# Performance work log

Measured on AMD Instinct MI355X. Metric: run time of the kernel, lower is better.

## Reference

```python
import jax, jax.numpy as jnp
import numpy as np

N, T, DYN, STAT, H = 50000, 24, 16, 8, 64
E = 1_600_000


def gru_last(x, Wih, Whh, bih, bhh):
    # x: [N, T, DYN]; torch GRU gate order: r, z, n
    gx = jnp.einsum('ntd,gd->ntg', x, Wih) + bih  # [N, T, 3H]
    h0 = jnp.zeros((x.shape[0], H), x.dtype)

    def step(h, gx_t):
        gh = h @ Whh.T + bhh  # [N, 3H]
        xr, xz, xn = jnp.split(gx_t, 3, axis=-1)
        hr, hz, hn = jnp.split(gh, 3, axis=-1)
        r = jax.nn.sigmoid(xr + hr)
        z = jax.nn.sigmoid(xz + hz)
        n = jnp.tanh(xn + r * hn)
        h_new = (1.0 - z) * n + z * h
        return h_new, None

    h_last, _ = jax.lax.scan(step, h0, jnp.swapaxes(gx, 0, 1))  # scan over T
    return h_last  # [N, H]


def gcn_layer(x, W, b, src, dst, w):
    h = x @ W  # [N, out]
    msg = h[src] * w[:, None]  # gather + weight  [E, out]
    agg = jax.ops.segment_sum(msg, dst, num_segments=N)  # scatter-add
    return agg + b


def setup_inputs() -> dict:
    key = jax.random.key(0)
    ks = jax.random.split(key, 16)
    s = 0.1
    return {
        'x_dyn': jax.random.normal(ks[0], (N, T, DYN), jnp.float32),
        'x_stat': jax.random.normal(ks[1], (N, STAT), jnp.float32),
        'edge_index': jax.random.randint(ks[2], (2, E), 0, N, jnp.int32),
        'edge_weight': jax.random.uniform(ks[3], (E,), jnp.float32),
        'Wih': jax.random.normal(ks[4], (3 * H, DYN), jnp.float32) * s,
        'Whh': jax.random.normal(ks[5], (3 * H, H), jnp.float32) * s,
        'bih': jnp.zeros((3 * H,), jnp.float32),
        'bhh': jnp.zeros((3 * H,), jnp.float32),
        'W1': jax.random.normal(ks[6], (H + STAT, H), jnp.float32) * s,
        'b1': jnp.zeros((H,), jnp.float32),
        'W2': jax.random.normal(ks[7], (H, H), jnp.float32) * s,
        'b2': jnp.zeros((H,), jnp.float32),
        'Wa': jax.random.normal(ks[8], (H, 1), jnp.float32) * s,
        'ba': jnp.zeros((1,), jnp.float32),
        'Wp': jax.random.normal(ks[9], (H, 1), jnp.float32) * s,
        'bp': jnp.zeros((1,), jnp.float32),
    }


def reference(x_dyn, x_stat, edge_index, edge_weight,
              Wih, Whh, bih, bhh, W1, b1, W2, b2, Wa, ba, Wp, bp):
    src, dst = edge_index[0], edge_index[1]
    z = gru_last(x_dyn, Wih, Whh, bih, bhh)            # [N, H]
    h = jnp.concatenate([z, x_stat], axis=1)           # [N, H+STAT]
    h = jax.nn.relu(gcn_layer(h, W1, b1, src, dst, edge_weight))
    h = jax.nn.relu(gcn_layer(h, W2, b2, src, dst, edge_weight))
    # dropout omitted (eval mode)
    aqi = (h @ Wa + ba)[:, 0]
    pm = (h @ Wp + bp)[:, 0]
    return aqi, pm
```

## Files before the change

### kernel.cpp

```cpp
#include <hip/hip_runtime.h>
#include <cstdint>
#include <cstddef>

#define NNODES 50000
#define TT 24
#define DYNF 16
#define STATF 8
#define HDIM 64
#define NEDGES 1600000
#define NB 32
#define GRU_BLOCKS ((NNODES + NB - 1) / NB)
#define FILL_CHUNK 1024
#define FILL_CHUNKS ((NEDGES + FILL_CHUNK - 1) / FILL_CHUNK)
#define CAP 80
#define SLICE (NNODES / 8)
#define BINCAP 210000
#define STAGE 192

typedef __attribute__((ext_vector_type(8))) short bf16x8;
typedef __attribute__((ext_vector_type(4))) float f32x4;
typedef __attribute__((ext_vector_type(2))) float f32x2;
typedef __attribute__((ext_vector_type(2))) unsigned u32x2;

__device__ __forceinline__ unsigned short f2bf(float f) {
    unsigned u = __float_as_uint(f);
    u = (u + 0x7FFFu + ((u >> 16) & 1u)) >> 16;
    return (unsigned short)u;
}
__device__ __forceinline__ float bf2f(unsigned short s) {
    return __uint_as_float((unsigned)s << 16);
}
__device__ __forceinline__ bf16x8 cvt8(const float* __restrict__ p) {
    bf16x8 r;
    #pragma unroll
    for (int i = 0; i < 8; ++i) r[i] = (short)f2bf(p[i]);
    return r;
}
__device__ __forceinline__ bf16x8 zero8() {
    bf16x8 z;
    #pragma unroll
    for (int i = 0; i < 8; ++i) z[i] = 0;
    return z;
}
__device__ __forceinline__ float fast_tanh(float x) {
    float e = __expf(2.f * x);
    return 1.f - 2.f * __builtin_amdgcn_rcpf(e + 1.f);
}

__global__ __launch_bounds__(256, 4) void gru_fill_kernel(
    const float* __restrict__ x_dyn, const float* __restrict__ x_stat,
    const float* __restrict__ Wih, const float* __restrict__ Whh,
    const float* __restrict__ bih, const float* __restrict__ bhh,
    const float* __restrict__ W1, unsigned short* __restrict__ t1,
    const int* __restrict__ srcv, const int* __restrict__ dstv,
    const float* __restrict__ ew, int* __restrict__ binCnt,
    u32x2* __restrict__ bins)
{
    constexpr int S_H = 72;
    constexpr int S_X = 40;
    __shared__ short hbuf[2][NB * S_H];
    __shared__ short xbuf[2][NB * S_X];
    __shared__ u32x2 stg[8][STAGE];
    __shared__ int lcnt[8];
    __shared__ int gbase[8];

    const int tid = (int)threadIdx.x;

    if ((int)blockIdx.x >= GRU_BLOCKS) {
        const int fb = (int)blockIdx.x - GRU_BLOCKS;
        const int base = fb * FILL_CHUNK;
        if (tid < 8) lcnt[tid] = 0;
        __syncthreads();
        #pragma unroll
        for (int j = 0; j < FILL_CHUNK / 256; ++j) {
            const int e = base + j * 256 + tid;
            if (e < NEDGES) {
                const int d = __builtin_nontemporal_load(dstv + e);
                const int s = __builtin_nontemporal_load(srcv + e);
                const float we = __builtin_nontemporal_load(ew + e);
                const int b = d / SLICE;
                u32x2 rec;
                rec[0] = (unsigned)s | ((unsigned)f2bf(we) << 16);
                rec[1] = (unsigned)(d - b * SLICE);
                const int pos = atomicAdd(&lcnt[b], 1);
                if (pos < STAGE) {
                    stg[b][pos] = rec;
                } else {
                    const int gp = atomicAdd(&binCnt[b], 1);
                    if (gp < BINCAP) bins[(size_t)b * BINCAP + gp] = rec;
                }
            }
        }
        __syncthreads();
        if (tid < 8) {
            const int n = min(lcnt[tid], STAGE);
            gbase[tid] = atomicAdd(&binCnt[tid], n);
        }
        __syncthreads();
        #pragma unroll 1
        for (int b = 0; b < 8; ++b) {
            const int n = min(lcnt[b], STAGE);
            const int gb = gbase[b];
            for (int i = tid; i < n; i += 256)
                if (gb + i < BINCAP)
                    bins[(size_t)b * BINCAP + gb + i] = stg[b][i];
        }
        return;
    }

    const int lane = tid & 63;
    const int w = __builtin_amdgcn_readfirstlane(tid >> 6);
    const int col = lane & 15;
    const int quad = lane >> 4;
    const int node0 = (int)blockIdx.x * NB;

    bf16x8 Bh[3][2];
    bf16x8 Bx[3];
    #pragma unroll
    for (int g = 0; g < 3; ++g) {
        const int n = (w + g * 4) * 16 + col;
        #pragma unroll
        for (int kt = 0; kt < 2; ++kt)
            Bh[g][kt] = cvt8(Whh + (size_t)n * HDIM + kt * 32 + quad * 8);
        Bx[g] = (quad < 2) ? cvt8(Wih + (size_t)n * DYNF + quad * 8) : zero8();
    }

    const int jg = w * 16 + col;
    const float b_r  = bih[jg]        + bhh[jg];
    const float b_z  = bih[HDIM + jg] + bhh[HDIM + jg];
    const float b_xn = bih[2 * HDIM + jg];
    const float b_hn = bhh[2 * HDIM + jg];

    for (int i = tid; i < NB * S_H; i += 256) hbuf[0][i] = 0;

    auto stage_x = [&](int t, int b) {
        const int nd = tid >> 3, c = tid & 7;
        int node = node0 + nd;
        if (node >= NNODES) node = 0;
        const f32x2 v = __builtin_nontemporal_load(
            reinterpret_cast<const f32x2*>(
                x_dyn + (size_t)node * (TT * DYNF) + t * DYNF + c * 2));
        unsigned pk = (unsigned)f2bf(v[0]) | ((unsigned)f2bf(v[1]) << 16);
        *reinterpret_cast<unsigned*>(&xbuf[b][nd * S_X + c * 2]) = pk;
        *reinterpret_cast<unsigned*>(&xbuf[b][nd * S_X + 16 + c * 2]) = 0u;
    };
    stage_x(0, 0);

    float hprev[2][4];
    #pragma unroll
    for (int mt = 0; mt < 2; ++mt)
        #pragma unroll
        for (int r = 0; r < 4; ++r) hprev[mt][r] = 0.f;

    for (int t = 0; t < TT; ++t) {
        const int rb = t & 1;
        __syncthreads();

        f32x4 accr[2], accz[2], accnh[2], accnx[2];
        #pragma unroll
        for (int mt = 0; mt < 2; ++mt) {
            const int nd = mt * 16 + col;
            const bf16x8 a0 = *reinterpret_cast<const bf16x8*>(&hbuf[rb][nd * S_H + quad * 8]);
            const bf16x8 a1 = *reinterpret_cast<const bf16x8*>(&hbuf[rb][nd * S_H + 32 + quad * 8]);
            const bf16x8 ax = *reinterpret_cast<const bf16x8*>(&xbuf[rb][nd * S_X + quad * 8]);
            const f32x4 z4 = {0.f, 0.f, 0.f, 0.f};
            accr[mt]  = __builtin_amdgcn_mfma_f32_16x16x32_bf16(a0, Bh[0][0], z4, 0, 0, 0);
            accr[mt]  = __builtin_amdgcn_mfma_f32_16x16x32_bf16(a1, Bh[0][1], accr[mt], 0, 0, 0);
            accr[mt]  = __builtin_amdgcn_mfma_f32_16x16x32_bf16(ax, Bx[0],    accr[mt], 0, 0, 0);
            accz[mt]  = __builtin_amdgcn_mfma_f32_16x16x32_bf16(a0, Bh[1][0], z4, 0, 0, 0);
            accz[mt]  = __builtin_amdgcn_mfma_f32_16x16x32_bf16(a1, Bh[1][1], accz[mt], 0, 0, 0);
            accz[mt]  = __builtin_amdgcn_mfma_f32_16x16x32_bf16(ax, Bx[1],    accz[mt], 0, 0, 0);
            accnh[mt] = __builtin_amdgcn_mfma_f32_16x16x32_bf16(a0, Bh[2][0], z4, 0, 0, 0);
            accnh[mt] = __builtin_amdgcn_mfma_f32_16x16x32_bf16(a1, Bh[2][1], accnh[mt], 0, 0, 0);
            accnx[mt] = __builtin_amdgcn_mfma_f32_16x16x32_bf16(ax, Bx[2],    z4, 0, 0, 0);
        }

        if (t + 1 < TT) stage_x(t + 1, rb ^ 1);

        #pragma unroll
        for (int mt = 0; mt < 2; ++mt) {
            #pragma unroll
            for (int r = 0; r < 4; ++r) {
                const float dr = 1.f + __expf(-(accr[mt][r] + b_r));
                const float dz = 1.f + __expf(-(accz[mt][r] + b_z));
                const float q  = __builtin_amdgcn_rcpf(dr * dz);
                const float R  = q * dz;
                const float Z  = q * dr;
                const float Nn = fast_tanh(accnx[mt][r] + b_xn + R * (accnh[mt][r] + b_hn));
                const float hn = Nn + Z * (hprev[mt][r] - Nn);
                hprev[mt][r] = hn;
                hbuf[rb ^ 1][(mt * 16 + quad * 4 + r) * S_H + jg] = (short)f2bf(hn);
            }
        }
    }
    __syncthreads();

    bf16x8 Bw0, Bw1, Bw2;
    #pragma unroll
    for (int j = 0; j < 8; ++j) {
        Bw0[j] = (short)f2bf(W1[(size_t)(quad * 8 + j) * HDIM + jg]);
        Bw1[j] = (short)f2bf(W1[(size_t)(32 + quad * 8 + j) * HDIM + jg]);
    }
    if (quad == 0) {
        #pragma unroll
        for (int j = 0; j < 8; ++j)
            Bw2[j] = (short)f2bf(W1[(size_t)(HDIM + j) * HDIM + jg]);
    } else {
        Bw2 = zero8();
    }

    #pragma unroll
    for (int mt = 0; mt < 2; ++mt) {
        const int nd = mt * 16 + col;
        const bf16x8 a0 = *reinterpret_cast<const bf16x8*>(&hbuf[0][nd * S_H + quad * 8]);
        const bf16x8 a1 = *reinterpret_cast<const bf16x8*>(&hbuf[0][nd * S_H + 32 + quad * 8]);
        bf16x8 axs;
        if (quad == 0) {
            int node = node0 + nd;
            if (node >= NNODES) node = 0;
            axs = cvt8(x_stat + (size_t)node * STATF);
        } else {
            axs = zero8();
        }
        const f32x4 z4 = {0.f, 0.f, 0.f, 0.f};
        f32x4 aw;
        aw = __builtin_amdgcn_mfma_f32_16x16x32_bf16(a0, Bw0, z4, 0, 0, 0);
        aw = __builtin_amdgcn_mfma_f32_16x16x32_bf16(a1, Bw1, aw, 0, 0, 0);
        aw = __builtin_amdgcn_mfma_f32_16x16x32_bf16(axs, Bw2, aw, 0, 0, 0);
        #pragma unroll
        for (int r = 0; r < 4; ++r) {
            const int node = node0 + mt * 16 + quad * 4 + r;
            if (node < NNODES) t1[(size_t)node * HDIM + jg] = f2bf(aw[r]);
        }
    }
}

__global__ __launch_bounds__(256) void fill_scatter_kernel(
    const u32x2* __restrict__ bins, const int* __restrict__ binCnt,
    int* __restrict__ cursor, unsigned* __restrict__ csr)
{
    const int slice = (int)blockIdx.x & 7;
    const int sub   = (int)blockIdx.x >> 3;
    const int lo    = slice * SLICE;
    const int cnt   = min(binCnt[slice], BINCAP);
    const u32x2* __restrict__ mybin = bins + (size_t)slice * BINCAP;
    for (int i = sub * 256 + (int)threadIdx.x; i < cnt; i += 96 * 256) {
        const u32x2 r = __builtin_nontemporal_load(mybin + i);
        const int d = lo + (int)r[1];
        const int pos = atomicAdd(&cursor[d], 1);
        if (pos < CAP) csr[(size_t)d * CAP + pos] = r[0];
    }
}

__global__ __launch_bounds__(256) void gather_transform_kernel(
    const unsigned short* __restrict__ tsrc, const int* __restrict__ cursor,
    const unsigned* __restrict__ csr, const float* __restrict__ b1,
    const float* __restrict__ W2, unsigned short* __restrict__ out)
{
    __shared__ float aggL[16][68];
    const int tid  = (int)threadIdx.x;
    const int lane = tid & 63;
    const int w    = tid >> 6;
    const int q    = lane >> 4;
    const int f    = lane & 15;
    const int col  = lane & 15;
    const int quad = lane >> 4;
    const int node0 = (int)blockIdx.x * 16;
    const int jg = w * 16 + col;

    bf16x8 Bw0, Bw1;
    float bk0[8], bk1[8];
    #pragma unroll
    for (int j = 0; j < 8; ++j) {
        Bw0[j] = (short)f2bf(W2[(size_t)(quad * 8 + j) * HDIM + jg]);
        Bw1[j] = (short)f2bf(W2[(size_t)(32 + quad * 8 + j) * HDIM + jg]);
        bk0[j] = b1[quad * 8 + j];
        bk1[j] = b1[32 + quad * 8 + j];
    }

    for (int i = 0; i < 4; ++i) {
        const int nloc = w * 4 + i;
        const int node = node0 + nloc;
        const int beg = node * CAP;
        const int cnt = min(cursor[node], CAP);
        const int end = beg + cnt;
        float a0 = 0.f, a1 = 0.f, a2 = 0.f, a3 = 0.f;
        int p = beg;
        for (; p + 8 <= end; p += 8) {
            const unsigned e0 = csr[p + q];
            const unsigned e1 = csr[p + 4 + q];
            const u32x2 r0 = *reinterpret_cast<const u32x2*>(
                tsrc + (size_t)(e0 & 0xFFFFu) * HDIM + 4 * f);
            const u32x2 r1 = *reinterpret_cast<const u32x2*>(
                tsrc + (size_t)(e1 & 0xFFFFu) * HDIM + 4 * f);
            const float w0 = __uint_as_float(e0 & 0xFFFF0000u);
            const float w1 = __uint_as_float(e1 & 0xFFFF0000u);
            a0 += w0 * bf2f((unsigned short)(r0[0] & 0xFFFFu));
            a1 += w0 * bf2f((unsigned short)(r0[0] >> 16));
            a2 += w0 * bf2f((unsigned short)(r0[1] & 0xFFFFu));
            a3 += w0 * bf2f((unsigned short)(r0[1] >> 16));
            a0 += w1 * bf2f((unsigned short)(r1[0] & 0xFFFFu));
            a1 += w1 * bf2f((unsigned short)(r1[0] >> 16));
            a2 += w1 * bf2f((unsigned short)(r1[1] & 0xFFFFu));
            a3 += w1 * bf2f((unsigned short)(r1[1] >> 16));
        }
        if (p + 4 <= end) {
            const unsigned e0 = csr[p + q];
            const u32x2 r0 = *reinterpret_cast<const u32x2*>(
                tsrc + (size_t)(e0 & 0xFFFFu) * HDIM + 4 * f);
            const float w0 = __uint_as_float(e0 & 0xFFFF0000u);
            a0 += w0 * bf2f((unsigned short)(r0[0] & 0xFFFFu));
            a1 += w0 * bf2f((unsigned short)(r0[0] >> 16));
            a2 += w0 * bf2f((unsigned short)(r0[1] & 0xFFFFu));
            a3 += w0 * bf2f((unsigned short)(r0[1] >> 16));
            p += 4;
        }
        const int rem = end - p;
        if (q < rem) {
            const unsigned e0 = csr[p + q];
            const u32x2 r0 = *reinterpret_cast<const u32x2*>(
                tsrc + (size_t)(e0 & 0xFFFFu) * HDIM + 4 * f);
            const float w0 = __uint_as_float(e0 & 0xFFFF0000u);
            a0 += w0 * bf2f((unsigned short)(r0[0] & 0xFFFFu));
            a1 += w0 * bf2f((unsigned short)(r0[0] >> 16));
            a2 += w0 * bf2f((unsigned short)(r0[1] & 0xFFFFu));
            a3 += w0 * bf2f((unsigned short)(r0[1] >> 16));
        }
        a0 += __shfl_xor(a0, 16, 64); a0 += __shfl_xor(a0, 32, 64);
        a1 += __shfl_xor(a1, 16, 64); a1 += __shfl_xor(a1, 32, 64);
        a2 += __shfl_xor(a2, 16, 64); a2 += __shfl_xor(a2, 32, 64);
        a3 += __shfl_xor(a3, 16, 64); a3 += __shfl_xor(a3, 32, 64);
        if (lane < 16) {
            f32x4 o; o[0] = a0; o[1] = a1; o[2] = a2; o[3] = a3;
            *reinterpret_cast<f32x4*>(&aggL[nloc][4 * f]) = o;
        }
    }
    __syncthreads();

    bf16x8 fa0, fa1;
    #pragma unroll
    for (int j = 0; j < 8; ++j) {
        fa0[j] = (short)f2bf(fmaxf(aggL[col][quad * 8 + j] + bk0[j], 0.f));
        fa1[j] = (short)f2bf(fmaxf(aggL[col][32 + quad * 8 + j] + bk1[j], 0.f));
    }
    const f32x4 z4 = {0.f, 0.f, 0.f, 0.f};
    f32x4 aw;
    aw = __builtin_amdgcn_mfma_f32_16x16x32_bf16(fa0, Bw0, z4, 0, 0, 0);
    aw = __builtin_amdgcn_mfma_f32_16x16x32_bf16(fa1, Bw1, aw, 0, 0, 0);
    #pragma unroll
    for (int r = 0; r < 4; ++r)
        out[(size_t)(node0 + quad * 4 + r) * HDIM + jg] = f2bf(aw[r]);
}

__global__ __launch_bounds__(256) void gather_head_kernel(
    const unsigned short* __restrict__ tsrc, const int* __restrict__ cursor,
    const unsigned* __restrict__ csr,
    const float* __restrict__ b2, const float* __restrict__ Wa,
    const float* __restrict__ ba, const float* __restrict__ Wp,
    const float* __restrict__ bp, float* __restrict__ out)
{
    const int node = blockIdx.x * 4 + (threadIdx.x >> 6);
    const int lane = (int)threadIdx.x & 63;
    const int q = lane >> 4;
    const int f = lane & 15;
    if (node >= NNODES) return;
    const int beg = node * CAP;
    const int cnt = min(cursor[node], CAP);
    const int end = beg + cnt;
    float a0 = 0.f, a1 = 0.f, a2 = 0.f, a3 = 0.f;
    int p = beg;
    for (; p + 8 <= end; p += 8) {
        const unsigned e0 = csr[p + q];
        const unsigned e1 = csr[p + 4 + q];
        const u32x2 r0 = *reinterpret_cast<const u32x2*>(
            tsrc + (size_t)(e0 & 0xFFFFu) * HDIM + 4 * f);
        const u32x2 r1 = *reinterpret_cast<const u32x2*>(
            tsrc + (size_t)(e1 & 0xFFFFu) * HDIM + 4 * f);
        const float w0 = __uint_as_float(e0 & 0xFFFF0000u);
        const float w1 = __uint_as_float(e1 & 0xFFFF0000u);
        a0 += w0 * bf2f((unsigned short)(r0[0] & 0xFFFFu));
        a1 += w0 * bf2f((unsigned short)(r0[0] >> 16));
        a2 += w0 * bf2f((unsigned short)(r0[1] & 0xFFFFu));
        a3 += w0 * bf2f((unsigned short)(r0[1] >> 16));
        a0 += w1 * bf2f((unsigned short)(r1[0] & 0xFFFFu));
        a1 += w1 * bf2f((unsigned short)(r1[0] >> 16));
        a2 += w1 * bf2f((unsigned short)(r1[1] & 0xFFFFu));
        a3 += w1 * bf2f((unsigned short)(r1[1] >> 16));
    }
    if (p + 4 <= end) {
        const unsigned e0 = csr[p + q];
        const u32x2 r0 = *reinterpret_cast<const u32x2*>(
            tsrc + (size_t)(e0 & 0xFFFFu) * HDIM + 4 * f);
        const float w0 = __uint_as_float(e0 & 0xFFFF0000u);
        a0 += w0 * bf2f((unsigned short)(r0[0] & 0xFFFFu));
        a1 += w0 * bf2f((unsigned short)(r0[0] >> 16));
        a2 += w0 * bf2f((unsigned short)(r0[1] & 0xFFFFu));
        a3 += w0 * bf2f((unsigned short)(r0[1] >> 16));
        p += 4;
    }
    const int rem = end - p;
    if (q < rem) {
        const unsigned e0 = csr[p + q];
        const u32x2 r0 = *reinterpret_cast<const u32x2*>(
            tsrc + (size_t)(e0 & 0xFFFFu) * HDIM + 4 * f);
        const float w0 = __uint_as_float(e0 & 0xFFFF0000u);
        a0 += w0 * bf2f((unsigned short)(r0[0] & 0xFFFFu));
        a1 += w0 * bf2f((unsigned short)(r0[0] >> 16));
        a2 += w0 * bf2f((unsigned short)(r0[1] & 0xFFFFu));
        a3 += w0 * bf2f((unsigned short)(r0[1] >> 16));
    }
    a0 += __shfl_xor(a0, 16, 64); a0 += __shfl_xor(a0, 32, 64);
    a1 += __shfl_xor(a1, 16, 64); a1 += __shfl_xor(a1, 32, 64);
    a2 += __shfl_xor(a2, 16, 64); a2 += __shfl_xor(a2, 32, 64);
    a3 += __shfl_xor(a3, 16, 64); a3 += __shfl_xor(a3, 32, 64);

    const f32x4 bb = *reinterpret_cast<const f32x4*>(b2 + 4 * f);
    const f32x4 wa = *reinterpret_cast<const f32x4*>(Wa + 4 * f);
    const f32x4 wp = *reinterpret_cast<const f32x4*>(Wp + 4 * f);
    const float h0 = fmaxf(a0 + bb[0], 0.f);
    const float h1 = fmaxf(a1 + bb[1], 0.f);
    const float h2 = fmaxf(a2 + bb[2], 0.f);
    const float h3 = fmaxf(a3 + bb[3], 0.f);
    float sa = h0 * wa[0] + h1 * wa[1] + h2 * wa[2] + h3 * wa[3];
    float sp = h0 * wp[0] + h1 * wp[1] + h2 * wp[2] + h3 * wp[3];
    #pragma unroll
    for (int off = 1; off < 16; off <<= 1) {
        sa += __shfl_xor(sa, off, 64);
        sp += __shfl_xor(sp, off, 64);
    }
    if (lane == 0) {
        out[node] = sa + ba[0];
        out[NNODES + node] = sp + bp[0];
    }
}

extern "C" void kernel_launch(void* const* d_in, const int* in_sizes, int n_in,
                              void* d_out, int out_size, void* d_ws, size_t ws_size,
                              hipStream_t stream)
{
    const float* x_dyn  = (const float*)d_in[0];
    const float* x_stat = (const float*)d_in[1];
    const int*   eidx   = (const int*)  d_in[2];
    const float* ew     = (const float*)d_in[3];
    const float* Wih    = (const float*)d_in[4];
    const float* Whh    = (const float*)d_in[5];
    const float* bih    = (const float*)d_in[6];
    const float* bhh    = (const float*)d_in[7];
    const float* W1     = (const float*)d_in[8];
    const float* b1     = (const float*)d_in[9];
    const float* W2     = (const float*)d_in[10];
    const float* b2     = (const float*)d_in[11];
    const float* Wa     = (const float*)d_in[12];
    const float* ba     = (const float*)d_in[13];
    const float* Wp     = (const float*)d_in[14];
    const float* bp     = (const float*)d_in[15];

    const int* srcv = eidx;
    const int* dstv = eidx + NEDGES;

    unsigned short* t1 = (unsigned short*)d_ws;
    unsigned short* t2 = t1 + (size_t)NNODES * HDIM;
    unsigned* csr = (unsigned*)(t2 + (size_t)NNODES * HDIM);
    int* cursor = (int*)(csr + (size_t)NNODES * CAP);
    int* binCnt = cursor + NNODES;
    u32x2* bins = (u32x2*)(binCnt + 16);

    dim3 blk(256);

    hipMemsetAsync(cursor, 0, (size_t)(NNODES + 16) * sizeof(int), stream);

    gru_fill_kernel<<<dim3(GRU_BLOCKS + FILL_CHUNKS), blk, 0, stream>>>(
        x_dyn, x_stat, Wih, Whh, bih, bhh, W1, t1,
        srcv, dstv, ew, binCnt, bins);

    fill_scatter_kernel<<<dim3(8 * 96), blk, 0, stream>>>(
        bins, binCnt, cursor, csr);

    gather_transform_kernel<<<dim3(NNODES / 16), blk, 0, stream>>>(
        t1, cursor, csr, b1, W2, t2);

    gather_head_kernel<<<dim3((NNODES + 3) / 4), blk, 0, stream>>>(
        t2, cursor, csr, b2, Wa, ba, Wp, bp, (float*)d_out);
}
```

Baseline: 376.9 us.

## Overlap CSR scatter with GRU and interleave four nodes per wave in gathers

The edge binning now runs as its own kernel first. The per-node CSR scatter is fused into the GRU kernel as extra blocks, so the scatter overlaps the recurrent compute instead of the binning. Both gather kernels now handle four nodes per wave at once, issuing four independent csr and feature loads per iteration to hide latency. This costs some wasted lanes on inactive nodes and more registers, and the head kernel now processes 16 nodes per block.

```diff
diff --git a/kernel.cpp b/kernel.cpp
--- a/kernel.cpp
+++ b/kernel.cpp
@@ -16,6 +16,7 @@
 #define SLICE (NNODES / 8)
 #define BINCAP 210000
 #define STAGE 192
+#define SCAT_BLOCKS 768
 
 typedef __attribute__((ext_vector_type(8))) short bf16x8;
 typedef __attribute__((ext_vector_type(4))) float f32x4;
@@ -47,63 +48,81 @@
     return 1.f - 2.f * __builtin_amdgcn_rcpf(e + 1.f);
 }
 
-__global__ __launch_bounds__(256, 4) void gru_fill_kernel(
+__global__ __launch_bounds__(256) void fill_bin_kernel(
+    const int* __restrict__ srcv, const int* __restrict__ dstv,
+    const float* __restrict__ ew, int* __restrict__ binCnt,
+    u32x2* __restrict__ bins)
+{
+    __shared__ u32x2 stg[8][STAGE];
+    __shared__ int lcnt[8];
+    __shared__ int gbase[8];
+    const int tid = (int)threadIdx.x;
+    const int base = (int)blockIdx.x * FILL_CHUNK;
+    if (tid < 8) lcnt[tid] = 0;
+    __syncthreads();
+    #pragma unroll
+    for (int j = 0; j < FILL_CHUNK / 256; ++j) {
+        const int e = base + j * 256 + tid;
+        if (e < NEDGES) {
+            const int d = __builtin_nontemporal_load(dstv + e);
+            const int s = __builtin_nontemporal_load(srcv + e);
+            const float we = __builtin_nontemporal_load(ew + e);
+            const int b = d / SLICE;
+            u32x2 rec;
+            rec[0] = (unsigned)s | ((unsigned)f2bf(we) << 16);
+            rec[1] = (unsigned)(d - b * SLICE);
+            const int pos = atomicAdd(&lcnt[b], 1);
+            if (pos < STAGE) {
+                stg[b][pos] = rec;
+            } else {
+                const int gp = atomicAdd(&binCnt[b], 1);
+                if (gp < BINCAP) bins[(size_t)b * BINCAP + gp] = rec;
+            }
+        }
+    }
+    __syncthreads();
+    if (tid < 8) {
+        const int n = min(lcnt[tid], STAGE);
+        gbase[tid] = atomicAdd(&binCnt[tid], n);
+    }
+    __syncthreads();
+    #pragma unroll 1
+    for (int b = 0; b < 8; ++b) {
+        const int n = min(lcnt[b], STAGE);
+        const int gb = gbase[b];
+        for (int i = tid; i < n; i += 256)
+            if (gb + i < BINCAP)
+                bins[(size_t)b * BINCAP + gb + i] = stg[b][i];
+    }
+}
+
+__global__ __launch_bounds__(256, 4) void gru_scatter_kernel(
     const float* __restrict__ x_dyn, const float* __restrict__ x_stat,
     const float* __restrict__ Wih, const float* __restrict__ Whh,
     const float* __restrict__ bih, const float* __restrict__ bhh,
     const float* __restrict__ W1, unsigned short* __restrict__ t1,
-    const int* __restrict__ srcv, const int* __restrict__ dstv,
-    const float* __restrict__ ew, int* __restrict__ binCnt,
-    u32x2* __restrict__ bins)
+    const u32x2* __restrict__ bins, const int* __restrict__ binCnt,
+    int* __restrict__ cursor, unsigned* __restrict__ csr)
 {
     constexpr int S_H = 72;
     constexpr int S_X = 40;
     __shared__ short hbuf[2][NB * S_H];
     __shared__ short xbuf[2][NB * S_X];
-    __shared__ u32x2 stg[8][STAGE];
-    __shared__ int lcnt[8];
-    __shared__ int gbase[8];
 
     const int tid = (int)threadIdx.x;
 
     if ((int)blockIdx.x >= GRU_BLOCKS) {
         const int fb = (int)blockIdx.x - GRU_BLOCKS;
-        const int base = fb * FILL_CHUNK;
-        if (tid < 8) lcnt[tid] = 0;
-        __syncthreads();
-        #pragma unroll
-        for (int j = 0; j < FILL_CHUNK / 256; ++j) {
-            const int e = base + j * 256 + tid;
-            if (e < NEDGES) {
-                const int d = __builtin_nontemporal_load(dstv + e);
-                const int s = __builtin_nontemporal_load(srcv + e);
-                const float we = __builtin_nontemporal_load(ew + e);
-                const int b = d / SLICE;
-                u32x2 rec;
-                rec[0] = (unsigned)s | ((unsigned)f2bf(we) << 16);
-                rec[1] = (unsigned)(d - b * SLICE);
-                const int pos = atomicAdd(&lcnt[b], 1);
-                if (pos < STAGE) {
-                    stg[b][pos] = rec;
-                } else {
-                    const int gp = atomicAdd(&binCnt[b], 1);
-                    if (gp < BINCAP) bins[(size_t)b * BINCAP + gp] = rec;
-                }
-            }
-        }
-        __syncthreads();
-        if (tid < 8) {
-            const int n = min(lcnt[tid], STAGE);
-            gbase[tid] = atomicAdd(&binCnt[tid], n);
-        }
-        __syncthreads();
-        #pragma unroll 1
-        for (int b = 0; b < 8; ++b) {
-            const int n = min(lcnt[b], STAGE);
-            const int gb = gbase[b];
-            for (int i = tid; i < n; i += 256)
-                if (gb + i < BINCAP)
-                    bins[(size_t)b * BINCAP + gb + i] = stg[b][i];
+        const int slice = fb & 7;
+        const int sub   = fb >> 3;
+        const int lo    = slice * SLICE;
+        const int cnt   = min(binCnt[slice], BINCAP);
+        const u32x2* __restrict__ mybin = bins + (size_t)slice * BINCAP;
+        for (int i = sub * 256 + tid; i < cnt; i += (SCAT_BLOCKS / 8) * 256) {
+            const u32x2 r = __builtin_nontemporal_load(mybin + i);
+            const int d = lo + (int)r[1];
+            const int pos = atomicAdd(&cursor[d], 1);
+            if (pos < CAP) csr[(size_t)d * CAP + pos] = r[0];
         }
         return;
     }
@@ -235,23 +254,6 @@
     }
 }
 
-__global__ __launch_bounds__(256) void fill_scatter_kernel(
-    const u32x2* __restrict__ bins, const int* __restrict__ binCnt,
-    int* __restrict__ cursor, unsigned* __restrict__ csr)
-{
-    const int slice = (int)blockIdx.x & 7;
-    const int sub   = (int)blockIdx.x >> 3;
-    const int lo    = slice * SLICE;
-    const int cnt   = min(binCnt[slice], BINCAP);
-    const u32x2* __restrict__ mybin = bins + (size_t)slice * BINCAP;
-    for (int i = sub * 256 + (int)threadIdx.x; i < cnt; i += 96 * 256) {
-        const u32x2 r = __builtin_nontemporal_load(mybin + i);
-        const int d = lo + (int)r[1];
-        const int pos = atomicAdd(&cursor[d], 1);
-        if (pos < CAP) csr[(size_t)d * CAP + pos] = r[0];
-    }
-}
-
 __global__ __launch_bounds__(256) void gather_transform_kernel(
     const unsigned short* __restrict__ tsrc, const int* __restrict__ cursor,
     const unsigned* __restrict__ csr, const float* __restrict__ b1,
@@ -263,76 +265,74 @@
     const int w    = tid >> 6;
     const int q    = lane >> 4;
     const int f    = lane & 15;
-    const int col  = lane & 15;
-    const int quad = lane >> 4;
     const int node0 = (int)blockIdx.x * 16;
-    const int jg = w * 16 + col;
+    const int jg = w * 16 + f;
 
     bf16x8 Bw0, Bw1;
     float bk0[8], bk1[8];
     #pragma unroll
     for (int j = 0; j < 8; ++j) {
-        Bw0[j] = (short)f2bf(W2[(size_t)(quad * 8 + j) * HDIM + jg]);
-        Bw1[j] = (short)f2bf(W2[(size_t)(32 + quad * 8 + j) * HDIM + jg]);
-        bk0[j] = b1[quad * 8 + j];
-        bk1[j] = b1[32 + quad * 8 + j];
-    }
-
-    for (int i = 0; i < 4; ++i) {
-        const int nloc = w * 4 + i;
-        const int node = node0 + nloc;
-        const int beg = node * CAP;
+        Bw0[j] = (short)f2bf(W2[(size_t)(q * 8 + j) * HDIM + jg]);
+        Bw1[j] = (short)f2bf(W2[(size_t)(32 + q * 8 + j) * HDIM + jg]);
+        bk0[j] = b1[q * 8 + j];
+        bk1[j] = b1[32 + q * 8 + j];
+    }
+
+    int pn[4], en[4], bg[4];
+    float a[4][4];
+    #pragma unroll
+    for (int n = 0; n < 4; ++n) {
+        const int node = node0 + w * 4 + n;
+        bg[n] = node * CAP;
         const int cnt = min(cursor[node], CAP);
-        const int end = beg + cnt;
-        float a0 = 0.f, a1 = 0.f, a2 = 0.f, a3 = 0.f;
-        int p = beg;
-        for (; p + 8 <= end; p += 8) {
-            const unsigned e0 = csr[p + q];
-            const unsigned e1 = csr[p + 4 + q];
-            const u32x2 r0 = *reinterpret_cast<const u32x2*>(
-                tsrc + (size_t)(e0 & 0xFFFFu) * HDIM + 4 * f);
-            const u32x2 r1 = *reinterpret_cast<const u32x2*>(
-                tsrc + (size_t)(e1 & 0xFFFFu) * HDIM + 4 * f);
-            const float w0 = __uint_as_float(e0 & 0xFFFF0000u);
-            const float w1 = __uint_as_float(e1 & 0xFFFF0000u);
-            a0 += w0 * bf2f((unsigned short)(r0[0] & 0xFFFFu));
-            a1 += w0 * bf2f((unsigned short)(r0[0] >> 16));
-            a2 += w0 * bf2f((unsigned short)(r0[1] & 0xFFFFu));
-            a3 += w0 * bf2f((unsigned short)(r0[1] >> 16));
-            a0 += w1 * bf2f((unsigned short)(r1[0] & 0xFFFFu));
-            a1 += w1 * bf2f((unsigned short)(r1[0] >> 16));
-            a2 += w1 * bf2f((unsigned short)(r1[1] & 0xFFFFu));
-            a3 += w1 * bf2f((unsigned short)(r1[1] >> 16));
-        }
-        if (p + 4 <= end) {
-            const unsigned e0 = csr[p + q];
-            const u32x2 r0 = *reinterpret_cast<const u32x2*>(
-                tsrc + (size_t)(e0 & 0xFFFFu) * HDIM + 4 * f);
-            const float w0 = __uint_as_float(e0 & 0xFFFF0000u);
-            a0 += w0 * bf2f((unsigned short)(r0[0] & 0xFFFFu));
-            a1 += w0 * bf2f((unsigned short)(r0[0] >> 16));
-            a2 += w0 * bf2f((unsigned short)(r0[1] & 0xFFFFu));
-            a3 += w0 * bf2f((unsigned short)(r0[1] >> 16));
-            p += 4;
-        }
-        const int rem = end - p;
-        if (q < rem) {
-            const unsigned e0 = csr[p + q];
-            const u32x2 r0 = *reinterpret_cast<const u32x2*>(
-                tsrc + (size_t)(e0 & 0xFFFFu) * HDIM + 4 * f);
-            const float w0 = __uint_as_float(e0 & 0xFFFF0000u);
-            a0 += w0 * bf2f((unsigned short)(r0[0] & 0xFFFFu));
-            a1 += w0 * bf2f((unsigned short)(r0[0] >> 16));
-            a2 += w0 * bf2f((unsigned short)(r0[1] & 0xFFFFu));
-            a3 += w0 * bf2f((unsigned short)(r0[1] >> 16));
-        }
-        a0 += __shfl_xor(a0, 16, 64); a0 += __shfl_xor(a0, 32, 64);
-        a1 += __shfl_xor(a1, 16, 64); a1 += __shfl_xor(a1, 32, 64);
-        a2 += __shfl_xor(a2, 16, 64); a2 += __shfl_xor(a2, 32, 64);
-        a3 += __shfl_xor(a3, 16, 64); a3 += __shfl_xor(a3, 32, 64);
-        if (lane < 16) {
-            f32x4 o; o[0] = a0; o[1] = a1; o[2] = a2; o[3] = a3;
-            *reinterpret_cast<f32x4*>(&aggL[nloc][4 * f]) = o;
+        pn[n] = bg[n] + q;
+        en[n] = bg[n] + cnt;
+        #pragma unroll
+        for (int j = 0; j < 4; ++j) a[n][j] = 0.f;
+    }
+
+    bool more = (pn[0] < en[0]) | (pn[1] < en[1]) |
+                (pn[2] < en[2]) | (pn[3] < en[3]);
+    while (__any(more)) {
+        bool act[4];
+        unsigned e[4];
+        #pragma unroll
+        for (int n = 0; n < 4; ++n) {
+            act[n] = pn[n] < en[n];
+            e[n] = csr[act[n] ? pn[n] : bg[n]];
+        }
+        u32x2 r[4];
+        #pragma unroll
+        for (int n = 0; n < 4; ++n) {
+            const int src = act[n] ? (int)(e[n] & 0xFFFFu) : 0;
+            r[n] = *reinterpret_cast<const u32x2*>(
+                tsrc + (size_t)src * HDIM + 4 * f);
+        }
+        #pragma unroll
+        for (int n = 0; n < 4; ++n) {
+            const float wg = act[n] ? __uint_as_float(e[n] & 0xFFFF0000u) : 0.f;
+            a[n][0] += wg * bf2f((unsigned short)(r[n][0] & 0xFFFFu));
+            a[n][1] += wg * bf2f((unsigned short)(r[n][0] >> 16));
+            a[n][2] += wg * bf2f((unsigned short)(r[n][1] & 0xFFFFu));
+            a[n][3] += wg * bf2f((unsigned short)(r[n][1] >> 16));
+            pn[n] += 4;
+        }
+        more = (pn[0] < en[0]) | (pn[1] < en[1]) |
+               (pn[2] < en[2]) | (pn[3] < en[3]);
+    }
+
+    #pragma unroll
+    for (int n = 0; n < 4; ++n)
+        #pragma unroll
+        for (int j = 0; j < 4; ++j) {
+            a[n][j] += __shfl_xor(a[n][j], 16, 64);
+            a[n][j] += __shfl_xor(a[n][j], 32, 64);
+        }
+    if (lane < 16) {
+        #pragma unroll
+        for (int n = 0; n < 4; ++n) {
+            f32x4 o; o[0] = a[n][0]; o[1] = a[n][1]; o[2] = a[n][2]; o[3] = a[n][3];
+            *reinterpret_cast<f32x4*>(&aggL[w * 4 + n][4 * f]) = o;
         }
     }
     __syncthreads();
@@ -340,8 +340,8 @@
     bf16x8 fa0, fa1;
     #pragma unroll
     for (int j = 0; j < 8; ++j) {
-        fa0[j] = (short)f2bf(fmaxf(aggL[col][quad * 8 + j] + bk0[j], 0.f));
-        fa1[j] = (short)f2bf(fmaxf(aggL[col][32 + quad * 8 + j] + bk1[j], 0.f));
+        fa0[j] = (short)f2bf(fmaxf(aggL[f][q * 8 + j] + bk0[j], 0.f));
+        fa1[j] = (short)f2bf(fmaxf(aggL[f][32 + q * 8 + j] + bk1[j], 0.f));
     }
     const f32x4 z4 = {0.f, 0.f, 0.f, 0.f};
     f32x4 aw;
@@ -349,7 +349,7 @@
     aw = __builtin_amdgcn_mfma_f32_16x16x32_bf16(fa1, Bw1, aw, 0, 0, 0);
     #pragma unroll
     for (int r = 0; r < 4; ++r)
-        out[(size_t)(node0 + quad * 4 + r) * HDIM + jg] = f2bf(aw[r]);
+        out[(size_t)(node0 + q * 4 + r) * HDIM + jg] = f2bf(aw[r]);
 }
 
 __global__ __launch_bounds__(256) void gather_head_kernel(
@@ -359,78 +359,89 @@
     const float* __restrict__ ba, const float* __restrict__ Wp,
     const float* __restrict__ bp, float* __restrict__ out)
 {
-    const int node = blockIdx.x * 4 + (threadIdx.x >> 6);
-    const int lane = (int)threadIdx.x & 63;
-    const int q = lane >> 4;
-    const int f = lane & 15;
-    if (node >= NNODES) return;
-    const int beg = node * CAP;
-    const int cnt = min(cursor[node], CAP);
-    const int end = beg + cnt;
-    float a0 = 0.f, a1 = 0.f, a2 = 0.f, a3 = 0.f;
-    int p = beg;
-    for (; p + 8 <= end; p += 8) {
-        const unsigned e0 = csr[p + q];
-        const unsigned e1 = csr[p + 4 + q];
-        const u32x2 r0 = *reinterpret_cast<const u32x2*>(
-            tsrc + (size_t)(e0 & 0xFFFFu) * HDIM + 4 * f);
-        const u32x2 r1 = *reinterpret_cast<const u32x2*>(
-            tsrc + (size_t)(e1 & 0xFFFFu) * HDIM + 4 * f);
-        const float w0 = __uint_as_float(e0 & 0xFFFF0000u);
-        const float w1 = __uint_as_float(e1 & 0xFFFF0000u);
-        a0 += w0 * bf2f((unsigned short)(r0[0] & 0xFFFFu));
-        a1 += w0 * bf2f((unsigned short)(r0[0] >> 16));
-        a2 += w0 * bf2f((unsigned short)(r0[1] & 0xFFFFu));
-        a3 += w0 * bf2f((unsigned short)(r0[1] >> 16));
-        a0 += w1 * bf2f((unsigned short)(r1[0] & 0xFFFFu));
-        a1 += w1 * bf2f((unsigned short)(r1[0] >> 16));
-        a2 += w1 * bf2f((unsigned short)(r1[1] & 0xFFFFu));
-        a3 += w1 * bf2f((unsigned short)(r1[1] >> 16));
-    }
-    if (p + 4 <= end) {
-        const unsigned e0 = csr[p + q];
-        const u32x2 r0 = *reinterpret_cast<const u32x2*>(
-            tsrc + (size_t)(e0 & 0xFFFFu) * HDIM + 4 * f);
-        const float w0 = __uint_as_float(e0 & 0xFFFF0000u);
-        a0 += w0 * bf2f((unsigned short)(r0[0] & 0xFFFFu));
-        a1 += w0 * bf2f((unsigned short)(r0[0] >> 16));
-        a2 += w0 * bf2f((unsigned short)(r0[1] & 0xFFFFu));
-        a3 += w0 * bf2f((unsigned short)(r0[1] >> 16));
-        p += 4;
-    }
-    const int rem = end - p;
-    if (q < rem) {
-        const unsigned e0 = csr[p + q];
-        const u32x2 r0 = *reinterpret_cast<const u32x2*>(
-            tsrc + (size_t)(e0 & 0xFFFFu) * HDIM + 4 * f);
-        const float w0 = __uint_as_float(e0 & 0xFFFF0000u);
-        a0 += w0 * bf2f((unsigned short)(r0[0] & 0xFFFFu));
-        a1 += w0 * bf2f((unsigned short)(r0[0] >> 16));
-        a2 += w0 * bf2f((unsigned short)(r0[1] & 0xFFFFu));
-        a3 += w0 * bf2f((unsigned short)(r0[1] >> 16));
-    }
-    a0 += __shfl_xor(a0, 16, 64); a0 += __shfl_xor(a0, 32, 64);
-    a1 += __shfl_xor(a1, 16, 64); a1 += __shfl_xor(a1, 32, 64);
-    a2 += __shfl_xor(a2, 16, 64); a2 += __shfl_xor(a2, 32, 64);
-    a3 += __shfl_xor(a3, 16, 64); a3 += __shfl_xor(a3, 32, 64);
+    const int tid  = (int)threadIdx.x;
+    const int lane = tid & 63;
+    const int w    = tid >> 6;
+    const int q    = lane >> 4;
+    const int f    = lane & 15;
+    const int node0 = (int)blockIdx.x * 16;
+
+    int pn[4], en[4], bg[4];
+    float a[4][4];
+    #pragma unroll
+    for (int n = 0; n < 4; ++n) {
+        const int node = node0 + w * 4 + n;
+        bg[n] = node * CAP;
+        const int cnt = min(cursor[node], CAP);
+        pn[n] = bg[n] + q;
+        en[n] = bg[n] + cnt;
+        #pragma unroll
+        for (int j = 0; j < 4; ++j) a[n][j] = 0.f;
+    }
+
+    bool more = (pn[0] < en[0]) | (pn[1] < en[1]) |
+                (pn[2] < en[2]) | (pn[3] < en[3]);
+    while (__any(more)) {
+        bool act[4];
+        unsigned e[4];
+        #pragma unroll
+        for (int n = 0; n < 4; ++n) {
+            act[n] = pn[n] < en[n];
+            e[n] = csr[act[n] ? pn[n] : bg[n]];
+        }
+        u32x2 r[4];
+        #pragma unroll
+        for (int n = 0; n < 4; ++n) {
+            const int src = act[n] ? (int)(e[n] & 0xFFFFu) : 0;
+            r[n] = *reinterpret_cast<const u32x2*>(
+                tsrc + (size_t)src * HDIM + 4 * f);
+        }
+        #pragma unroll
+        for (int n = 0; n < 4; ++n) {
+            const float wg = act[n] ? __uint_as_float(e[n] & 0xFFFF0000u) : 0.f;
+            a[n][0] += wg * bf2f((unsigned short)(r[n][0] & 0xFFFFu));
+            a[n][1] += wg * bf2f((unsigned short)(r[n][0] >> 16));
+            a[n][2] += wg * bf2f((unsigned short)(r[n][1] & 0xFFFFu));
+            a[n][3] += wg * bf2f((unsigned short)(r[n][1] >> 16));
+            pn[n] += 4;
+        }
+        more = (pn[0] < en[0]) | (pn[1] < en[1]) |
+               (pn[2] < en[2]) | (pn[3] < en[3]);
+    }
+
+    #pragma unroll
+    for (int n = 0; n < 4; ++n)
+        #pragma unroll
+        for (int j = 0; j < 4; ++j) {
+            a[n][j] += __shfl_xor(a[n][j], 16, 64);
+            a[n][j] += __shfl_xor(a[n][j], 32, 64);
+        }
 
     const f32x4 bb = *reinterpret_cast<const f32x4*>(b2 + 4 * f);
     const f32x4 wa = *reinterpret_cast<const f32x4*>(Wa + 4 * f);
     const f32x4 wp = *reinterpret_cast<const f32x4*>(Wp + 4 * f);
-    const float h0 = fmaxf(a0 + bb[0], 0.f);
-    const float h1 = fmaxf(a1 + bb[1], 0.f);
-    const float h2 = fmaxf(a2 + bb[2], 0.f);
-    const float h3 = fmaxf(a3 + bb[3], 0.f);
-    float sa = h0 * wa[0] + h1 * wa[1] + h2 * wa[2] + h3 * wa[3];
-    float sp = h0 * wp[0] + h1 * wp[1] + h2 * wp[2] + h3 * wp[3];
-    #pragma unroll
-    for (int off = 1; off < 16; off <<= 1) {
-        sa += __shfl_xor(sa, off, 64);
-        sp += __shfl_xor(sp, off, 64);
+    float sa[4], sp[4];
+    #pragma unroll
+    for (int n = 0; n < 4; ++n) {
+        const float h0 = fmaxf(a[n][0] + bb[0], 0.f);
+        const float h1 = fmaxf(a[n][1] + bb[1], 0.f);
+        const float h2 = fmaxf(a[n][2] + bb[2], 0.f);
+        const float h3 = fmaxf(a[n][3] + bb[3], 0.f);
+        sa[n] = h0 * wa[0] + h1 * wa[1] + h2 * wa[2] + h3 * wa[3];
+        sp[n] = h0 * wp[0] + h1 * wp[1] + h2 * wp[2] + h3 * wp[3];
+        #pragma unroll
+        for (int off = 1; off < 16; off <<= 1) {
+            sa[n] += __shfl_xor(sa[n], off, 64);
+            sp[n] += __shfl_xor(sp[n], off, 64);
+        }
     }
     if (lane == 0) {
-        out[node] = sa + ba[0];
-        out[NNODES + node] = sp + bp[0];
+        #pragma unroll
+        for (int n = 0; n < 4; ++n) {
+            const int node = node0 + w * 4 + n;
+            out[node] = sa[n] + ba[0];
+            out[NNODES + node] = sp[n] + bp[0];
+        }
     }
 }
 
@@ -469,16 +480,16 @@
 
     hipMemsetAsync(cursor, 0, (size_t)(NNODES + 16) * sizeof(int), stream);
 
-    gru_fill_kernel<<<dim3(GRU_BLOCKS + FILL_CHUNKS), blk, 0, stream>>>(
+    fill_bin_kernel<<<dim3(FILL_CHUNKS), blk, 0, stream>>>(
+        srcv, dstv, ew, binCnt, bins);
+
+    gru_scatter_kernel<<<dim3(GRU_BLOCKS + SCAT_BLOCKS), blk, 0, stream>>>(
         x_dyn, x_stat, Wih, Whh, bih, bhh, W1, t1,
-        srcv, dstv, ew, binCnt, bins);
-
-    fill_scatter_kernel<<<dim3(8 * 96), blk, 0, stream>>>(
         bins, binCnt, cursor, csr);
 
     gather_transform_kernel<<<dim3(NNODES / 16), blk, 0, stream>>>(
         t1, cursor, csr, b1, W2, t2);
 
-    gather_head_kernel<<<dim3((NNODES + 3) / 4), blk, 0, stream>>>(
+    gather_head_kernel<<<dim3(NNODES / 16), blk, 0, stream>>>(
         t2, cursor, csr, b2, Wa, ba, Wp, bp, (float*)d_out);
 }
```

Result: faster. 343.5 us (median of 2 runs) (-8.9%).
